# Performance work log

Hardware: AMD Instinct MI355X
Metric: run time of the kernel (lower is better)

The kernel has to match this reference:

```python
import jax, jax.numpy as jnp
import numpy as np

EPS = 1e-5  # BatchNorm2d default eps


def _bn_params(c, gamma):
    # rows: gamma, beta, running_mean, running_var (inference-mode BN)
    return jnp.stack([jnp.full((c,), gamma, jnp.float32),
                      jnp.zeros((c,), jnp.float32),
                      jnp.zeros((c,), jnp.float32),
                      jnp.ones((c,), jnp.float32)])


def _bn(x, p):
    g, b, m, v = p
    scale = (g / jnp.sqrt(v + EPS)).reshape(1, -1, 1, 1)
    return (x - m.reshape(1, -1, 1, 1)) * scale + b.reshape(1, -1, 1, 1)


def _conv1x1(x, w, b):
    # w: [O, C]; 1x1 Conv2d == channel matmul
    return jnp.einsum('oc,nctv->notv', w, x) + b[None, :, None, None]


def setup_inputs() -> dict:
    key = jax.random.key(0)
    N, C, COUT, T, V, S = 8, 64, 128, 256, 256, 3
    IC = COUT // 4  # coff_embedding = 4
    ks = jax.random.split(key, 10)
    rn = lambda k, shp, s=0.05: jax.random.normal(k, shp, jnp.float32) * s
    x = jax.random.normal(ks[0], (N, C, T, V), jnp.float32)
    mat_adj = jax.random.uniform(ks[1], (S, T, T), jnp.float32) * (1.0 / T)  # static adjacency
    adj_weight = jnp.full((S, T, T), 1e-6, jnp.float32)  # nn.init.constant_(weight, 1e-6)
    return {
        'x': x,
        'mat_adj': mat_adj,
        'adj_weight': adj_weight,
        'wa': rn(ks[2], (S, IC, C)), 'ba': jnp.zeros((S, IC), jnp.float32),
        'wb': rn(ks[3], (S, IC, C)), 'bb': jnp.zeros((S, IC), jnp.float32),
        'wd': rn(ks[4], (S, COUT, C)), 'bd': jnp.zeros((S, COUT), jnp.float32),
        'gcn_bn': _bn_params(COUT, 1e-6),  # util.init_bn(self.bn, 1e-6)
        'cres_w': rn(ks[5], (COUT, C)), 'cres_b': jnp.zeros((COUT,), jnp.float32),
        'cres_bn': _bn_params(COUT, 1.0),
        'tcn_w': rn(ks[6], (COUT, COUT, 9)), 'tcn_b': jnp.zeros((COUT,), jnp.float32),
        'tcn_bn': _bn_params(COUT, 1.0),
        'rt_w': rn(ks[7], (COUT, C)), 'rt_b': jnp.zeros((COUT,), jnp.float32),
        'rt_bn': _bn_params(COUT, 1.0),
    }


def reference(x, mat_adj, adj_weight, wa, ba, wb, bb, wd, bd, gcn_bn,
              cres_w, cres_b, cres_bn, tcn_w, tcn_b, tcn_bn, rt_w, rt_b, rt_bn):
    N, C, T, V = x.shape
    A = mat_adj + adj_weight  # [S, T, T]
    y = 0.0
    for i in range(A.shape[0]):  # num_subset = 3, structurally distinct weights
        a = _conv1x1(x, wa[i], ba[i])      # [N, IC, T, V]
        be = _conv1x1(x, wb[i], bb[i])     # [N, IC, T, V]
        # embed1 [N,T,IC*V] @ embed2 [N,IC*V,T] -> contract over (IC, V)
        scores = jnp.einsum('nctv,ncsv->nts', a, be) / V
        att = jax.nn.softmax(scores, axis=-2)  # Softmax(dim=-2)
        adapt = A[i] + att                      # [N, T, T]
        # mat_inpt [N,C*V,T] @ adapt -> view(N,C,V,T)
        xa = jnp.einsum('nctv,nts->ncvs', x, adapt)  # [N, C, V, T]
        y = y + _conv1x1(xa, wd[i], bd[i])           # [N, COUT, V, T]
    gcn = jax.nn.relu(_bn(y, gcn_bn) + _bn(_conv1x1(x, cres_w, cres_b), cres_bn))
    # UnitTSCN: Conv2d kernel (9,1), stride (1,1), padding (4,0), then BN
    t = jax.lax.conv_general_dilated(gcn, tcn_w[..., None], (1, 1), ((4, 4), (0, 0)),
                                     dimension_numbers=('NCHW', 'OIHW', 'NCHW'))
    t = _bn(t + tcn_b[None, :, None, None], tcn_bn)
    # residual path: UnitTSCN(kernel_size=1, stride=1) since in != out
    r = _bn(_conv1x1(x, rt_w, rt_b), rt_bn)
    return jax.nn.relu(t + r)
```

## Files before the change

### kernel.cpp

```cpp
#include <hip/hip_runtime.h>

typedef unsigned short u16;

#define DEVI static __device__ __forceinline__

DEVI float bf2f(u16 v) { return __uint_as_float(((unsigned)v) << 16); }
DEVI u16 f2bf(float f) {
  unsigned u = __float_as_uint(f);
  u += 0x7FFFu + ((u >> 16) & 1u);
  return (u16)(u >> 16);
}
DEVI unsigned pk2bf(float a, float b) {
  unsigned r;
  asm("v_cvt_pk_bf16_f32 %0, %1, %2" : "=v"(r) : "v"(a), "v"(b));
  return r;
}

typedef __attribute__((ext_vector_type(8))) short short8;
typedef __attribute__((ext_vector_type(4))) float floatx4;

#define GSWZ(q, g) (((q) << 6) + ((((g) ^ ((q) & 7) ^ (((q) >> 3) & 7))) << 3))


__global__ void k_diag(float* out, float v) { out[0] = v; }

__global__ __launch_bounds__(256) void k_xt(
    const float* __restrict__ x, u16* __restrict__ xt)
{
  __shared__ __align__(16) u16 Ls[256 * 64];
  const int n = blockIdx.z, c = blockIdx.y, t0 = blockIdx.x << 6;
  const int tid = threadIdx.x;
  const float* xp = x + (((size_t)(n << 6) + c) << 16);
  const int t4 = (tid & 15) << 2;
  #pragma unroll
  for (int j = 0; j < 4; ++j) {
    const int v4 = ((tid >> 4) << 2) + (j << 6);
    float4 f0 = *(const float4*)(xp + ((t0 + t4 + 0) << 8) + v4);
    float4 f1 = *(const float4*)(xp + ((t0 + t4 + 1) << 8) + v4);
    float4 f2 = *(const float4*)(xp + ((t0 + t4 + 2) << 8) + v4);
    float4 f3 = *(const float4*)(xp + ((t0 + t4 + 3) << 8) + v4);
    const float fr[4][4] = {{f0.x,f1.x,f2.x,f3.x},{f0.y,f1.y,f2.y,f3.y},
                            {f0.z,f1.z,f2.z,f3.z},{f0.w,f1.w,f2.w,f3.w}};
    #pragma unroll
    for (int dv = 0; dv < 4; ++dv) {
      int v = v4 + dv;
      unsigned p0 = pk2bf(fr[dv][0], fr[dv][1]);
      unsigned p1 = pk2bf(fr[dv][2], fr[dv][3]);
      int e = (v << 6) + (((t4 >> 3) ^ (v & 7)) << 3) + (t4 & 4);
      *(uint2*)&Ls[e] = make_uint2(p0, p1);
    }
  }
  __syncthreads();
  const int g = tid & 7;
  u16* xo = xt + (((size_t)((n << 6) + c)) << 16) + t0;
  #pragma unroll
  for (int it = 0; it < 8; ++it) {
    int v = (tid >> 3) + (it << 5);
    short8 row = *(const short8*)&Ls[(v << 6) + ((g ^ (v & 7)) << 3)];
    *(short8*)(xo + (v << 8) + (g << 3)) = row;
  }
}

__global__ __launch_bounds__(256) void k_ab2(
    const float* __restrict__ x, const float* __restrict__ wa, const float* __restrict__ ba,
    const float* __restrict__ wb, const float* __restrict__ bb,
    u16* __restrict__ a_buf, u16* __restrict__ b_buf, int sub)
{
  __shared__ __align__(16) u16 Aw[64 * 64];
  __shared__ __align__(16) u16 Bx[256 * 64];
  __shared__ float sbias[64];
  const int n = blockIdx.y;
  const int q0 = blockIdx.x << 8;
  const int tid = threadIdx.x;

  if (tid < 64) sbias[tid] = (tid < 32) ? ba[sub * 32 + tid] : bb[sub * 32 + tid - 32];
  {
    const int kq = tid & 15;
    const int rr = tid >> 4;
    #pragma unroll
    for (int j = 0; j < 4; ++j) {
      int r = rr + (j << 4);
      float4 wv = (r < 32) ? *(const float4*)(wa + sub * 2048 + r * 64 + (kq << 2))
                           : *(const float4*)(wb + sub * 2048 + (r - 32) * 64 + (kq << 2));
      int e = (r << 6) + (((kq >> 1) ^ (r & 7)) << 3) + ((kq & 1) << 2);
      *(uint2*)&Aw[e] = make_uint2(pk2bf(wv.x, wv.y), pk2bf(wv.z, wv.w));
    }
  }
  {
    const int q4 = (tid & 63) << 2;
    const int kb = (tid >> 6) << 4;
    #pragma unroll
    for (int half = 0; half < 2; ++half) {
      float fa[8][4];
      #pragma unroll
      for (int dk = 0; dk < 8; ++dk)
        *(float4*)fa[dk] = *(const float4*)(x + (((size_t)(n << 6) + kb + half * 8 + dk) << 16) + q0 + q4);
      const int G = (kb >> 3) + half;
      #pragma unroll
      for (int dq = 0; dq < 4; ++dq) {
        unsigned w0 = pk2bf(fa[0][dq], fa[1][dq]);
        unsigned w1 = pk2bf(fa[2][dq], fa[3][dq]);
        unsigned w2 = pk2bf(fa[4][dq], fa[5][dq]);
        unsigned w3 = pk2bf(fa[6][dq], fa[7][dq]);
        *(uint4*)&Bx[GSWZ(q4 + dq, G)] = make_uint4(w0, w1, w2, w3);
      }
    }
  }
  __syncthreads();

  const int lane = tid & 63, wave = tid >> 6;
  const int qw = wave << 6;
  const int l15 = lane & 15, lg = lane >> 4;
  int aoff[4], boff[4];
  #pragma unroll
  for (int m = 0; m < 4; ++m) { int r = (m << 4) + l15; aoff[m] = (r << 6) + ((r & 7) << 3); }
  #pragma unroll
  for (int nn = 0; nn < 4; ++nn) { int q = qw + (nn << 4) + l15; boff[nn] = GSWZ(q, 0); }

  floatx4 acc[4][4];
  #pragma unroll
  for (int m = 0; m < 4; ++m)
    #pragma unroll
    for (int nn = 0; nn < 4; ++nn) acc[m][nn] = (floatx4){0.f, 0.f, 0.f, 0.f};

  #pragma unroll
  for (int ks = 0; ks < 2; ++ks) {
    const int gs = ((ks << 2) + lg) << 3;
    short8 av[4], bv[4];
    #pragma unroll
    for (int m = 0; m < 4; ++m) av[m] = *(const short8*)&Aw[aoff[m] ^ gs];
    #pragma unroll
    for (int nn = 0; nn < 4; ++nn) bv[nn] = *(const short8*)&Bx[boff[nn] ^ gs];
    #pragma unroll
    for (int m = 0; m < 4; ++m)
      #pragma unroll
      for (int nn = 0; nn < 4; ++nn)
        acc[m][nn] = __builtin_amdgcn_mfma_f32_16x16x32_bf16(av[m], bv[nn], acc[m][nn], 0, 0, 0);
  }

  #pragma unroll
  for (int m = 0; m < 4; ++m) {
    #pragma unroll
    for (int r = 0; r < 4; ++r) {
      int row = (m << 4) + (lg << 2) + r;
      float bias = sbias[row];
      u16* dst = (row < 32) ? a_buf + (((n * 32 + row) << 16) + q0)
                            : b_buf + (((n * 32 + row - 32) << 16) + q0);
      #pragma unroll
      for (int np = 0; np < 2; ++np) {
        unsigned p = pk2bf(acc[m][2 * np][r] + bias, acc[m][2 * np + 1][r] + bias);
        dst[qw + np * 32 + l15] = (u16)p;
        dst[qw + np * 32 + 16 + l15] = (u16)(p >> 16);
      }
    }
  }
}

__global__ __launch_bounds__(256) void k_sc2(
    const u16* __restrict__ a_buf, const u16* __restrict__ b_buf,
    float* __restrict__ part)
{
  __shared__ __align__(16) u16 At[128 * 64];
  __shared__ __align__(16) u16 Bt[128 * 64];
  const int n = blockIdx.z;
  const int kg = blockIdx.y;
  const int t0 = (blockIdx.x >> 1) << 7;
  const int s0 = (blockIdx.x & 1) << 7;
  const int tid = threadIdx.x;
  const int lane = tid & 63, wave = tid >> 6;
  const int tw = (wave & 1) << 6;
  const int sw = (wave >> 1) << 6;
  const int l15 = lane & 15, lg = lane >> 4;
  const int g = tid & 7;
  const int trow = tid >> 3;

  int aoff[4], boff[4];
  #pragma unroll
  for (int m = 0; m < 4; ++m) { int t = tw + (m << 4) + l15; aoff[m] = (t << 6) + ((t & 7) << 3); }
  #pragma unroll
  for (int nn = 0; nn < 4; ++nn) { int s = sw + (nn << 4) + l15; boff[nn] = (s << 6) + ((s & 7) << 3); }

  floatx4 acc[4][4];
  #pragma unroll
  for (int m = 0; m < 4; ++m)
    #pragma unroll
    for (int nn = 0; nn < 4; ++nn) acc[m][nn] = (floatx4){0.f, 0.f, 0.f, 0.f};

  for (int cc = 0; cc < 4; ++cc) {
    const int c = (kg << 2) + cc;
    const u16* ap = a_buf + ((n * 32 + c) << 16);
    const u16* bp = b_buf + ((n * 32 + c) << 16);
    for (int vt = 0; vt < 4; ++vt) {
      const int v0 = vt << 6;
      __syncthreads();
      #pragma unroll
      for (int j = 0; j < 4; ++j) {
        int t = trow + (j << 5);
        int e = (t << 6) + ((g ^ (t & 7)) << 3);
        *(short8*)&At[e] = *(const short8*)(ap + (t0 + t) * 256 + v0 + g * 8);
        *(short8*)&Bt[e] = *(const short8*)(bp + (s0 + t) * 256 + v0 + g * 8);
      }
      __syncthreads();
      #pragma unroll
      for (int ks = 0; ks < 2; ++ks) {
        const int gs = ((ks << 2) + lg) << 3;
        short8 av[4], bv[4];
        #pragma unroll
        for (int m = 0; m < 4; ++m) av[m] = *(const short8*)&At[aoff[m] ^ gs];
        #pragma unroll
        for (int nn = 0; nn < 4; ++nn) bv[nn] = *(const short8*)&Bt[boff[nn] ^ gs];
        #pragma unroll
        for (int m = 0; m < 4; ++m)
          #pragma unroll
          for (int nn = 0; nn < 4; ++nn)
            acc[m][nn] = __builtin_amdgcn_mfma_f32_16x16x32_bf16(av[m], bv[nn], acc[m][nn], 0, 0, 0);
      }
    }
  }

  const float inv256 = 1.0f / 256.0f;
  float* pp = part + (((kg << 3) + n) << 16);
  #pragma unroll
  for (int m = 0; m < 4; ++m) {
    #pragma unroll
    for (int r = 0; r < 4; ++r) {
      int t = t0 + tw + (m << 4) + (lg << 2) + r;
      #pragma unroll
      for (int nn = 0; nn < 4; ++nn) {
        int s = s0 + sw + (nn << 4) + l15;
        pp[t * 256 + s] = acc[m][nn][r] * inv256;
      }
    }
  }
}

__global__ __launch_bounds__(256) void k_soft2(
    const float* __restrict__ part, const float* __restrict__ madj,
    const float* __restrict__ wadj, float* __restrict__ adapt, int sub)
{
  __shared__ float Ls[256][32];
  __shared__ float redm[8][32];
  __shared__ float reds[8][32];
  const int sc = blockIdx.x;
  const int n = blockIdx.y;
  const int tid = threadIdx.x;
  const int sl = tid & 31, tg = tid >> 5;
  const int s = (sc << 5) + sl;

  float m = -1e30f;
  for (int i = 0; i < 32; ++i) {
    int t = (tg << 5) + i;
    int off = t * 256 + s;
    float v = 0.f;
    #pragma unroll
    for (int k = 0; k < 8; ++k) v += part[(((k << 3) + n) << 16) + off];
    Ls[t][sl] = v;
    m = fmaxf(m, v);
  }
  redm[tg][sl] = m;
  __syncthreads();
  #pragma unroll
  for (int k = 0; k < 8; ++k) m = fmaxf(m, redm[k][sl]);
  float sum = 0.f;
  for (int i = 0; i < 32; ++i) {
    int t = (tg << 5) + i;
    sum += __expf(Ls[t][sl] - m);
  }
  reds[tg][sl] = sum;
  __syncthreads();
  float tot = 0.f;
  #pragma unroll
  for (int k = 0; k < 8; ++k) tot += reds[k][sl];
  float inv = 1.0f / tot;
  const float* ma = madj + (sub << 16);
  const float* wa2 = wadj + (sub << 16);
  float* adp = adapt + (n << 16);
  for (int i = 0; i < 32; ++i) {
    int t = (tg << 5) + i;
    int off = t * 256 + s;
    adp[off] = __expf(Ls[t][sl] - m) * inv + ma[off] + wa2[off];
  }
}

__global__ __launch_bounds__(256) void k_xa2(
    const u16* __restrict__ xt, const float* __restrict__ adapt,
    u16* __restrict__ xa)
{
  __shared__ __align__(16) u16 Av[128 * 64];
  __shared__ __align__(16) u16 Bt2[128 * 64];
  const int n = blockIdx.z, c = blockIdx.y;
  const int v0 = (blockIdx.x >> 1) << 7;
  const int s0 = (blockIdx.x & 1) << 7;
  const int tid = threadIdx.x;
  const int lane = tid & 63, wave = tid >> 6;
  const int vw = (wave & 1) << 6, sw = (wave >> 1) << 6;
  const int l15 = lane & 15, lg = lane >> 4;
  const int ga = tid & 7, vr = tid >> 3;
  const int q4 = (tid & 31) << 2, kb = (tid >> 5) << 3;
  const u16* xp = xt + (((size_t)((n << 6) + c)) << 16);
  const float* ap = adapt + (n << 16);

  int aoff[4], boff[4];
  #pragma unroll
  for (int m = 0; m < 4; ++m) { int v = vw + (m << 4) + l15; aoff[m] = (v << 6) + ((v & 7) << 3); }
  #pragma unroll
  for (int nn = 0; nn < 4; ++nn) { int s = sw + (nn << 4) + l15; boff[nn] = GSWZ(s, 0); }

  floatx4 acc[4][4];
  #pragma unroll
  for (int m = 0; m < 4; ++m)
    #pragma unroll
    for (int nn = 0; nn < 4; ++nn) acc[m][nn] = (floatx4){0.f, 0.f, 0.f, 0.f};

  for (int kt = 0; kt < 4; ++kt) {
    const int tb = kt << 6;
    __syncthreads();
    #pragma unroll
    for (int j = 0; j < 4; ++j) {
      int v = vr + (j << 5);
      *(short8*)&Av[(v << 6) + ((ga ^ (v & 7)) << 3)] =
        *(const short8*)(xp + ((v0 + v) << 8) + tb + (ga << 3));
    }
    {
      float fa[8][4];
      #pragma unroll
      for (int dk = 0; dk < 8; ++dk)
        *(float4*)fa[dk] = *(const float4*)(ap + ((tb + kb + dk) << 8) + s0 + q4);
      const int G = kb >> 3;
      #pragma unroll
      for (int dq = 0; dq < 4; ++dq) {
        unsigned w0 = pk2bf(fa[0][dq], fa[1][dq]);
        unsigned w1 = pk2bf(fa[2][dq], fa[3][dq]);
        unsigned w2 = pk2bf(fa[4][dq], fa[5][dq]);
        unsigned w3 = pk2bf(fa[6][dq], fa[7][dq]);
        *(uint4*)&Bt2[GSWZ(q4 + dq, G)] = make_uint4(w0, w1, w2, w3);
      }
    }
    __syncthreads();
    #pragma unroll
    for (int ks = 0; ks < 2; ++ks) {
      const int gs = ((ks << 2) + lg) << 3;
      short8 av[4], bv[4];
      #pragma unroll
      for (int m = 0; m < 4; ++m) av[m] = *(const short8*)&Av[aoff[m] ^ gs];
      #pragma unroll
      for (int nn = 0; nn < 4; ++nn) bv[nn] = *(const short8*)&Bt2[boff[nn] ^ gs];
      #pragma unroll
      for (int m = 0; m < 4; ++m)
        #pragma unroll
        for (int nn = 0; nn < 4; ++nn)
          acc[m][nn] = __builtin_amdgcn_mfma_f32_16x16x32_bf16(av[m], bv[nn], acc[m][nn], 0, 0, 0);
    }
  }

  u16* xo = xa + (((n << 6) + c) << 16);
  #pragma unroll
  for (int m = 0; m < 4; ++m) {
    #pragma unroll
    for (int r = 0; r < 4; ++r) {
      int v = v0 + vw + (m << 4) + (lg << 2) + r;
      u16* dst = xo + v * 256 + s0;
      #pragma unroll
      for (int np = 0; np < 2; ++np) {
        unsigned p = pk2bf(acc[m][2 * np][r], acc[m][2 * np + 1][r]);
        dst[sw + np * 32 + l15] = (u16)p;
        dst[sw + np * 32 + 16 + l15] = (u16)(p >> 16);
      }
    }
  }
}

__global__ __launch_bounds__(256) void k_gcnf(
    const u16* __restrict__ xa_all, const float* __restrict__ x,
    const float* __restrict__ wd, const float* __restrict__ bd,
    const float* __restrict__ cw, const float* __restrict__ cb,
    const float* __restrict__ cbn, const float* __restrict__ gbn,
    u16* __restrict__ gcn)
{
  __shared__ __align__(16) u16 Wt[128 * 64];
  __shared__ __align__(16) u16 Gt[128 * 64];
  __shared__ float s_kk[128], s_sg[128], s_sc[128];
  const int n = blockIdx.y;
  const int q0 = blockIdx.x << 7;
  const int tid = threadIdx.x;
  if (tid < 128) {
    int o = tid;
    float sg = gbn[o] * rsqrtf(gbn[384 + o] + 1e-5f);
    float sc = cbn[o] * rsqrtf(cbn[384 + o] + 1e-5f);
    s_sg[o] = sg; s_sc[o] = sc;
    s_kk[o] = sg * (bd[o] + bd[128 + o] + bd[256 + o])
            + (cb[o] - cbn[256 + o]) * sc + cbn[128 + o]
            - gbn[256 + o] * sg + gbn[128 + o];
  }
  __syncthreads();

  const int lane = tid & 63, wave = tid >> 6;
  const int ow = (wave & 1) << 6;
  const int qw = (wave >> 1) << 6;
  const int l15 = lane & 15, lg = lane >> 4;
  const int kq = tid & 15;
  const int orow = tid >> 4;
  const int q4 = (tid & 31) << 2;
  const int kb = (tid >> 5) << 3;

  int aoff[4], boff[4];
  #pragma unroll
  for (int m = 0; m < 4; ++m) { int o = ow + (m << 4) + l15; aoff[m] = (o << 6) + ((o & 7) << 3); }
  #pragma unroll
  for (int nn = 0; nn < 4; ++nn) { int q = qw + (nn << 4) + l15; boff[nn] = GSWZ(q, 0); }

  floatx4 acc[4][4];
  #pragma unroll
  for (int m = 0; m < 4; ++m)
    #pragma unroll
    for (int nn = 0; nn < 4; ++nn) acc[m][nn] = (floatx4){0.f, 0.f, 0.f, 0.f};

  for (int kt = 0; kt < 6; ++kt) {
    __syncthreads();
    #pragma unroll
    for (int j = 0; j < 8; ++j) {
      int o = orow + (j << 4);
      int e = (o << 6) + (((kq >> 1) ^ (o & 7)) << 3) + ((kq & 1) << 2);
      if (kt < 3) {
        float4 wv = *(const float4*)(wd + kt * 8192 + o * 64 + (kq << 2));
        float s = s_sg[o];
        *(uint2*)&Wt[e] = make_uint2(pk2bf(s * wv.x, s * wv.y), pk2bf(s * wv.z, s * wv.w));
      } else {
        float4 wv = *(const float4*)(cw + o * 64 + (kq << 2));
        float s = s_sc[o];
        float f0 = s * wv.x, f1 = s * wv.y, f2 = s * wv.z, f3 = s * wv.w;
        unsigned h01 = pk2bf(f0, f1), h23 = pk2bf(f2, f3);
        if (kt == 4) {
          float g0 = __uint_as_float(h01 << 16), g1 = __uint_as_float(h01 & 0xffff0000u);
          float g2 = __uint_as_float(h23 << 16), g3 = __uint_as_float(h23 & 0xffff0000u);
          *(uint2*)&Wt[e] = make_uint2(pk2bf(f0 - g0, f1 - g1), pk2bf(f2 - g2, f3 - g3));
        } else {
          *(uint2*)&Wt[e] = make_uint2(h01, h23);
        }
      }
    }
    if (kt != 4) {
      const int G = kb >> 3;
      if (kt < 3) {
        const u16* xp = xa_all + (size_t)kt * 33554432u + (((size_t)(n << 6) + kb) << 16);
        u16 va[8][4];
        #pragma unroll
        for (int dk = 0; dk < 8; ++dk) {
          ushort4 t4 = *(const ushort4*)(xp + ((size_t)dk << 16) + q0 + q4);
          va[dk][0] = t4.x; va[dk][1] = t4.y; va[dk][2] = t4.z; va[dk][3] = t4.w;
        }
        #pragma unroll
        for (int dq = 0; dq < 4; ++dq) {
          unsigned p0 = (unsigned)va[0][dq] | ((unsigned)va[1][dq] << 16);
          unsigned p1 = (unsigned)va[2][dq] | ((unsigned)va[3][dq] << 16);
          unsigned p2 = (unsigned)va[4][dq] | ((unsigned)va[5][dq] << 16);
          unsigned p3 = (unsigned)va[6][dq] | ((unsigned)va[7][dq] << 16);
          *(uint4*)&Gt[GSWZ(q4 + dq, G)] = make_uint4(p0, p1, p2, p3);
        }
      } else {
        float fa[8][4];
        #pragma unroll
        for (int dk = 0; dk < 8; ++dk)
          *(float4*)fa[dk] = *(const float4*)(x + (((size_t)(n << 6) + kb + dk) << 16) + q0 + q4);
        #pragma unroll
        for (int dq = 0; dq < 4; ++dq) {
          unsigned p[4];
          #pragma unroll
          for (int k2 = 0; k2 < 4; ++k2) {
            unsigned h = pk2bf(fa[2 * k2][dq], fa[2 * k2 + 1][dq]);
            if (kt == 5) {
              float g0 = __uint_as_float(h << 16), g1 = __uint_as_float(h & 0xffff0000u);
              h = pk2bf(fa[2 * k2][dq] - g0, fa[2 * k2 + 1][dq] - g1);
            }
            p[k2] = h;
          }
          *(uint4*)&Gt[GSWZ(q4 + dq, G)] = make_uint4(p[0], p[1], p[2], p[3]);
        }
      }
    }
    __syncthreads();
    #pragma unroll
    for (int ks = 0; ks < 2; ++ks) {
      const int gs = ((ks << 2) + lg) << 3;
      short8 av[4], bv[4];
      #pragma unroll
      for (int m = 0; m < 4; ++m) av[m] = *(const short8*)&Wt[aoff[m] ^ gs];
      #pragma unroll
      for (int nn = 0; nn < 4; ++nn) bv[nn] = *(const short8*)&Gt[boff[nn] ^ gs];
      #pragma unroll
      for (int m = 0; m < 4; ++m)
        #pragma unroll
        for (int nn = 0; nn < 4; ++nn)
          acc[m][nn] = __builtin_amdgcn_mfma_f32_16x16x32_bf16(av[m], bv[nn], acc[m][nn], 0, 0, 0);
    }
  }

  #pragma unroll
  for (int m = 0; m < 4; ++m) {
    #pragma unroll
    for (int r = 0; r < 4; ++r) {
      int o = ow + (m << 4) + (lg << 2) + r;
      float kadd = s_kk[o];
      u16* dst = gcn + (((n << 7) + o) << 16) + q0;
      #pragma unroll
      for (int np = 0; np < 2; ++np) {
        float v0 = fmaxf(acc[m][2 * np][r] + kadd, 0.f);
        float v1 = fmaxf(acc[m][2 * np + 1][r] + kadd, 0.f);
        unsigned p = pk2bf(v0, v1);
        dst[qw + np * 32 + l15] = (u16)p;
        dst[qw + np * 32 + 16 + l15] = (u16)(p >> 16);
      }
    }
  }
}

__global__ __launch_bounds__(256) void k_out(
    const u16* __restrict__ gcn, const float* __restrict__ x,
    const float* __restrict__ tw, const float* __restrict__ tb, const float* __restrict__ tbn,
    const float* __restrict__ rw, const float* __restrict__ rb, const float* __restrict__ rbn,
    float* __restrict__ out)
{
  __shared__ __align__(16) u16 Wh[128 * 64];
  __shared__ __align__(16) u16 Wl[128 * 64];
  __shared__ __align__(16) u16 Gc[128 * 64];
  __shared__ float s_st[128], s_sr[128], s_kk[128];
  const int n = blockIdx.y;
  const int q0 = blockIdx.x << 7;
  const int h = q0 >> 8;
  const int w0 = q0 & 255;
  const int tid = threadIdx.x;
  if (tid < 128) {
    int o = tid;
    float st = tbn[o] * rsqrtf(tbn[384 + o] + 1e-5f);
    float sr = rbn[o] * rsqrtf(rbn[384 + o] + 1e-5f);
    s_st[o] = st; s_sr[o] = sr;
    s_kk[o] = (tb[o] - tbn[256 + o]) * st + tbn[128 + o]
            + (rb[o] - rbn[256 + o]) * sr + rbn[128 + o];
  }
  __syncthreads();

  const int lane = tid & 63;
  const int wave = tid >> 6;
  const int ow = (wave & 1) << 6;
  const int qw = (wave >> 1) << 6;
  const int l15 = lane & 15;
  const int lg  = lane >> 4;

  const int kq   = tid & 15;
  const int orow = tid >> 4;
  const int q4   = (tid & 31) << 2;
  const int kb   = (tid >> 5) << 3;

  float stj[8], srj[8];
  #pragma unroll
  for (int j = 0; j < 8; ++j) { int o = orow + (j << 4); stj[j] = s_st[o]; srj[j] = s_sr[o]; }

  int aoff[4], boff[4];
  #pragma unroll
  for (int m = 0; m < 4; ++m) { int o = ow + (m << 4) + l15; aoff[m] = (o << 6) + ((o & 7) << 3); }
  #pragma unroll
  for (int nn = 0; nn < 4; ++nn) { int q = qw + (nn << 4) + l15; boff[nn] = GSWZ(q, 0); }

  floatx4 acc[4][4];
  #pragma unroll
  for (int m = 0; m < 4; ++m)
    #pragma unroll
    for (int nn = 0; nn < 4; ++nn)
      acc[m][nn] = (floatx4){0.f, 0.f, 0.f, 0.f};

  for (int kc = 0; kc < 19; ++kc) {
    __syncthreads();
    {
      const int k4 = (kc << 6) + (kq << 2);
      #pragma unroll
      for (int j = 0; j < 8; ++j) {
        int o = orow + (j << 4);
        float4 wv;
        float s;
        if (kc < 18) { wv = *(const float4*)(tw + o * 1152 + k4); s = stj[j]; }
        else         { wv = *(const float4*)(rw + (o << 6) + (k4 - 1152)); s = srj[j]; }
        float f0 = s * wv.x, f1 = s * wv.y, f2 = s * wv.z, f3 = s * wv.w;
        unsigned h01 = pk2bf(f0, f1), h23 = pk2bf(f2, f3);
        float g0 = __uint_as_float(h01 << 16), g1 = __uint_as_float(h01 & 0xffff0000u);
        float g2 = __uint_as_float(h23 << 16), g3 = __uint_as_float(h23 & 0xffff0000u);
        unsigned l01 = pk2bf(f0 - g0, f1 - g1), l23 = pk2bf(f2 - g2, f3 - g3);
        int e = (o << 6) + (((kq >> 1) ^ (o & 7)) << 3) + ((kq & 1) << 2);
        *(uint2*)&Wh[e] = make_uint2(h01, h23);
        *(uint2*)&Wl[e] = make_uint2(l01, l23);
      }
    }
    {
      const int G = kb >> 3;
      if (kc < 18) {
        u16 va[8][4];
        #pragma unroll
        for (int dk = 0; dk < 8; ++dk) {
          int k = (kc << 6) + kb + dk;
          unsigned i = (unsigned)k / 9u;
          int kh = k - 9 * (int)i;
          int h2 = h + kh - 4;
          ushort4 t4;
          if ((unsigned)h2 < 256u)
            t4 = *(const ushort4*)(gcn + ((((n << 7) + (int)i) << 16) + (h2 << 8) + w0 + q4));
          else t4 = make_ushort4(0, 0, 0, 0);
          va[dk][0] = t4.x; va[dk][1] = t4.y; va[dk][2] = t4.z; va[dk][3] = t4.w;
        }
        #pragma unroll
        for (int dq = 0; dq < 4; ++dq) {
          unsigned p0 = (unsigned)va[0][dq] | ((unsigned)va[1][dq] << 16);
          unsigned p1 = (unsigned)va[2][dq] | ((unsigned)va[3][dq] << 16);
          unsigned p2 = (unsigned)va[4][dq] | ((unsigned)va[5][dq] << 16);
          unsigned p3 = (unsigned)va[6][dq] | ((unsigned)va[7][dq] << 16);
          *(uint4*)&Gc[GSWZ(q4 + dq, G)] = make_uint4(p0, p1, p2, p3);
        }
      } else {
        float fa[8][4];
        #pragma unroll
        for (int dk = 0; dk < 8; ++dk)
          *(float4*)fa[dk] = *(const float4*)(x + (((size_t)(n << 6) + kb + dk) << 16) + q0 + q4);
        #pragma unroll
        for (int dq = 0; dq < 4; ++dq) {
          unsigned w0_ = pk2bf(fa[0][dq], fa[1][dq]);
          unsigned w1_ = pk2bf(fa[2][dq], fa[3][dq]);
          unsigned w2_ = pk2bf(fa[4][dq], fa[5][dq]);
          unsigned w3_ = pk2bf(fa[6][dq], fa[7][dq]);
          *(uint4*)&Gc[GSWZ(q4 + dq, G)] = make_uint4(w0_, w1_, w2_, w3_);
        }
      }
    }
    __syncthreads();
    #pragma unroll
    for (int ks = 0; ks < 2; ++ks) {
      const int gs = ((ks << 2) + lg) << 3;
      short8 ah[4], al[4], bg[4];
      #pragma unroll
      for (int m = 0; m < 4; ++m) {
        ah[m] = *(const short8*)&Wh[aoff[m] ^ gs];
        al[m] = *(const short8*)&Wl[aoff[m] ^ gs];
      }
      #pragma unroll
      for (int nn = 0; nn < 4; ++nn)
        bg[nn] = *(const short8*)&Gc[boff[nn] ^ gs];
      #pragma unroll
      for (int m = 0; m < 4; ++m)
        #pragma unroll
        for (int nn = 0; nn < 4; ++nn) {
          acc[m][nn] = __builtin_amdgcn_mfma_f32_16x16x32_bf16(ah[m], bg[nn], acc[m][nn], 0, 0, 0);
          acc[m][nn] = __builtin_amdgcn_mfma_f32_16x16x32_bf16(al[m], bg[nn], acc[m][nn], 0, 0, 0);
        }
    }
  }

  #pragma unroll
  for (int m = 0; m < 4; ++m) {
    #pragma unroll
    for (int r = 0; r < 4; ++r) {
      int o = ow + (m << 4) + (lg << 2) + r;
      float kadd = s_kk[o];
      float* dst = out + (((size_t)((n << 7) + o)) << 16) + q0;
      #pragma unroll
      for (int nn = 0; nn < 4; ++nn) {
        int q = qw + (nn << 4) + l15;
        dst[q] = fmaxf(acc[m][nn][r] + kadd, 0.f);
      }
    }
  }
}

extern "C" void kernel_launch(void* const* d_in, const int* in_sizes, int n_in,
                              void* d_out, int out_size, void* d_ws, size_t ws_size,
                              hipStream_t stream) {
  const float* x       = (const float*)d_in[0];
  const float* mat_adj = (const float*)d_in[1];
  const float* adj_w   = (const float*)d_in[2];
  const float* wa      = (const float*)d_in[3];
  const float* ba      = (const float*)d_in[4];
  const float* wb      = (const float*)d_in[5];
  const float* bb      = (const float*)d_in[6];
  const float* wd      = (const float*)d_in[7];
  const float* bd      = (const float*)d_in[8];
  const float* gcn_bn  = (const float*)d_in[9];
  const float* cres_w  = (const float*)d_in[10];
  const float* cres_b  = (const float*)d_in[11];
  const float* cres_bn = (const float*)d_in[12];
  const float* tcn_w   = (const float*)d_in[13];
  const float* tcn_b   = (const float*)d_in[14];
  const float* tcn_bn  = (const float*)d_in[15];
  const float* rt_w    = (const float*)d_in[16];
  const float* rt_b    = (const float*)d_in[17];
  const float* rt_bn   = (const float*)d_in[18];
  float* out = (float*)d_out;

  (void)hipGetLastError();

  hipMemsetAsync(d_out, 0x42, 4, stream);

  if (n_in != 19)                    { k_diag<<<1,1,0,stream>>>(out, 2019.f); return; }
  if (in_sizes[0]  != 33554432)      { k_diag<<<1,1,0,stream>>>(out, 2000.f); return; }
  if (in_sizes[3]  != 6144)          { k_diag<<<1,1,0,stream>>>(out, 2003.f); return; }
  if (in_sizes[7]  != 24576)         { k_diag<<<1,1,0,stream>>>(out, 2007.f); return; }
  if (in_sizes[9]  != 512)           { k_diag<<<1,1,0,stream>>>(out, 2009.f); return; }
  if (in_sizes[13] != 147456)        { k_diag<<<1,1,0,stream>>>(out, 2013.f); return; }
  if (in_sizes[16] != 8192)          { k_diag<<<1,1,0,stream>>>(out, 2016.f); return; }
  if (out_size != 67108864)          { k_diag<<<1,1,0,stream>>>(out, 3000.f); return; }
  if (ws_size < 134217728ull)        { k_diag<<<1,1,0,stream>>>(out, (float)ws_size); return; }

  float* wsf   = (float*)d_ws;
  u16*   a_buf = (u16*)d_ws;
  u16*   b_buf = a_buf + 16777216;
  float* part  = wsf + 16777216;
  float* adapt = wsf + 20971520;
  u16*   gcn   = (u16*)d_ws;
  u16*   xa_all = (u16*)d_out;
  u16*   x_t   = ((u16*)d_out) + 100663296;

  k_xt<<<dim3(4, 64, 8), 256, 0, stream>>>(x, x_t);
  for (int i = 0; i < 3; ++i) {
    k_ab2  <<<dim3(256, 8),   256, 0, stream>>>(x, wa, ba, wb, bb, a_buf, b_buf, i);
    k_sc2  <<<dim3(4, 8, 8),  256, 0, stream>>>(a_buf, b_buf, part);
    k_soft2<<<dim3(8, 8),     256, 0, stream>>>(part, mat_adj, adj_w, adapt, i);
    k_xa2  <<<dim3(4, 64, 8), 256, 0, stream>>>(x_t, adapt, xa_all + (size_t)i * 33554432u);
  }
  k_gcnf<<<dim3(512, 8), 256, 0, stream>>>(xa_all, x, wd, bd, cres_w, cres_b,
                                           cres_bn, gcn_bn, gcn);
  k_out<<<dim3(512, 8), 256, 0, stream>>>(gcn, x, tcn_w, tcn_b, tcn_bn,
                                          rt_w, rt_b, rt_bn, out);

  hipError_t le = hipGetLastError();
  if (le != hipSuccess) {
    k_diag<<<1, 1, 0, stream>>>(out, 1.0e9f + (float)(int)le);
  }
}
```

Baseline: 1.605 ms.

## Prefetch next k-chunk into registers in k_out and peel residual chunk

The temporal-conv output kernel now loads the next chunk's weights and gcn tile into registers while the current chunk is converted and multiplied. This is meant to hide global-memory latency behind the MFMA work. The residual 1x1 chunk is moved out of the main loop into its own epilogue step, removing the per-iteration branch. Launch bounds now ask for 3 blocks per CU. In exchange the prefetch buffers raise register pressure, and the hand-placed barriers with an explicit lgkmcnt wait replace the plain __syncthreads.

```diff
diff --git a/kernel.cpp b/kernel.cpp
--- a/kernel.cpp
+++ b/kernel.cpp
@@ -514,7 +514,7 @@
   }
 }
 
-__global__ __launch_bounds__(256) void k_out(
+__global__ __launch_bounds__(256, 3) void k_out(
     const u16* __restrict__ gcn, const float* __restrict__ x,
     const float* __restrict__ tw, const float* __restrict__ tb, const float* __restrict__ tbn,
     const float* __restrict__ rw, const float* __restrict__ rb, const float* __restrict__ rbn,
@@ -552,14 +552,19 @@
   const int kb   = (tid >> 5) << 3;
 
   float stj[8], srj[8];
-  #pragma unroll
-  for (int j = 0; j < 8; ++j) { int o = orow + (j << 4); stj[j] = s_st[o]; srj[j] = s_sr[o]; }
+  int weoff[8];
+  #pragma unroll
+  for (int j = 0; j < 8; ++j) {
+    int o = orow + (j << 4);
+    stj[j] = s_st[o]; srj[j] = s_sr[o];
+    weoff[j] = (o << 6) + (((kq >> 1) ^ (o & 7)) << 3) + ((kq & 1) << 2);
+  }
 
   int aoff[4], boff[4];
   #pragma unroll
   for (int m = 0; m < 4; ++m) { int o = ow + (m << 4) + l15; aoff[m] = (o << 6) + ((o & 7) << 3); }
   #pragma unroll
-  for (int nn = 0; nn < 4; ++nn) { int q = qw + (nn << 4) + l15; boff[nn] = GSWZ(q, 0); }
+  for (int nn = 0; nn < 4; ++nn) { int q = qw + (nn << 4) + l15; boff[nn] = (q << 6) + ((q & 7) << 3); }
 
   floatx4 acc[4][4];
   #pragma unroll
@@ -568,67 +573,71 @@
     for (int nn = 0; nn < 4; ++nn)
       acc[m][nn] = (floatx4){0.f, 0.f, 0.f, 0.f};
 
-  for (int kc = 0; kc < 19; ++kc) {
-    __syncthreads();
+  float4 wbuf[8];
+  ushort4 gbuf[8];
+
+  {
+    const int k4 = kq << 2;
+    #pragma unroll
+    for (int j = 0; j < 8; ++j)
+      wbuf[j] = *(const float4*)(tw + (orow + (j << 4)) * 1152 + k4);
+    #pragma unroll
+    for (int dk = 0; dk < 8; ++dk) {
+      int k = kb + dk;
+      unsigned i = (unsigned)k / 9u;
+      int kh = k - 9 * (int)i;
+      int h2 = h + kh - 4;
+      gbuf[dk] = ((unsigned)h2 < 256u)
+        ? *(const ushort4*)(gcn + ((((n << 7) + (int)i) << 16) + (h2 << 8) + w0 + q4))
+        : make_ushort4(0, 0, 0, 0);
+    }
+  }
+
+  for (int kc = 0; kc < 18; ++kc) {
+    __builtin_amdgcn_s_barrier();
+    #pragma unroll
+    for (int j = 0; j < 8; ++j) {
+      float s = stj[j];
+      float f0 = s * wbuf[j].x, f1 = s * wbuf[j].y, f2 = s * wbuf[j].z, f3 = s * wbuf[j].w;
+      u16 b0 = f2bf(f0), b1 = f2bf(f1), b2 = f2bf(f2), b3 = f2bf(f3);
+      *(ushort4*)&Wh[weoff[j]] = make_ushort4(b0, b1, b2, b3);
+      *(ushort4*)&Wl[weoff[j]] = make_ushort4(f2bf(f0 - bf2f(b0)), f2bf(f1 - bf2f(b1)),
+                                              f2bf(f2 - bf2f(b2)), f2bf(f3 - bf2f(b3)));
+    }
     {
-      const int k4 = (kc << 6) + (kq << 2);
-      #pragma unroll
-      for (int j = 0; j < 8; ++j) {
-        int o = orow + (j << 4);
-        float4 wv;
-        float s;
-        if (kc < 18) { wv = *(const float4*)(tw + o * 1152 + k4); s = stj[j]; }
-        else         { wv = *(const float4*)(rw + (o << 6) + (k4 - 1152)); s = srj[j]; }
-        float f0 = s * wv.x, f1 = s * wv.y, f2 = s * wv.z, f3 = s * wv.w;
-        unsigned h01 = pk2bf(f0, f1), h23 = pk2bf(f2, f3);
-        float g0 = __uint_as_float(h01 << 16), g1 = __uint_as_float(h01 & 0xffff0000u);
-        float g2 = __uint_as_float(h23 << 16), g3 = __uint_as_float(h23 & 0xffff0000u);
-        unsigned l01 = pk2bf(f0 - g0, f1 - g1), l23 = pk2bf(f2 - g2, f3 - g3);
-        int e = (o << 6) + (((kq >> 1) ^ (o & 7)) << 3) + ((kq & 1) << 2);
-        *(uint2*)&Wh[e] = make_uint2(h01, h23);
-        *(uint2*)&Wl[e] = make_uint2(l01, l23);
-      }
-    }
-    {
+      u16 va[8][4];
+      #pragma unroll
+      for (int dk = 0; dk < 8; ++dk) {
+        va[dk][0] = gbuf[dk].x; va[dk][1] = gbuf[dk].y;
+        va[dk][2] = gbuf[dk].z; va[dk][3] = gbuf[dk].w;
+      }
       const int G = kb >> 3;
-      if (kc < 18) {
-        u16 va[8][4];
-        #pragma unroll
-        for (int dk = 0; dk < 8; ++dk) {
-          int k = (kc << 6) + kb + dk;
-          unsigned i = (unsigned)k / 9u;
-          int kh = k - 9 * (int)i;
-          int h2 = h + kh - 4;
-          ushort4 t4;
-          if ((unsigned)h2 < 256u)
-            t4 = *(const ushort4*)(gcn + ((((n << 7) + (int)i) << 16) + (h2 << 8) + w0 + q4));
-          else t4 = make_ushort4(0, 0, 0, 0);
-          va[dk][0] = t4.x; va[dk][1] = t4.y; va[dk][2] = t4.z; va[dk][3] = t4.w;
-        }
-        #pragma unroll
-        for (int dq = 0; dq < 4; ++dq) {
-          unsigned p0 = (unsigned)va[0][dq] | ((unsigned)va[1][dq] << 16);
-          unsigned p1 = (unsigned)va[2][dq] | ((unsigned)va[3][dq] << 16);
-          unsigned p2 = (unsigned)va[4][dq] | ((unsigned)va[5][dq] << 16);
-          unsigned p3 = (unsigned)va[6][dq] | ((unsigned)va[7][dq] << 16);
-          *(uint4*)&Gc[GSWZ(q4 + dq, G)] = make_uint4(p0, p1, p2, p3);
-        }
-      } else {
-        float fa[8][4];
-        #pragma unroll
-        for (int dk = 0; dk < 8; ++dk)
-          *(float4*)fa[dk] = *(const float4*)(x + (((size_t)(n << 6) + kb + dk) << 16) + q0 + q4);
-        #pragma unroll
-        for (int dq = 0; dq < 4; ++dq) {
-          unsigned w0_ = pk2bf(fa[0][dq], fa[1][dq]);
-          unsigned w1_ = pk2bf(fa[2][dq], fa[3][dq]);
-          unsigned w2_ = pk2bf(fa[4][dq], fa[5][dq]);
-          unsigned w3_ = pk2bf(fa[6][dq], fa[7][dq]);
-          *(uint4*)&Gc[GSWZ(q4 + dq, G)] = make_uint4(w0_, w1_, w2_, w3_);
-        }
-      }
-    }
-    __syncthreads();
+      #pragma unroll
+      for (int dq = 0; dq < 4; ++dq) {
+        int q = q4 + dq;
+        int e = (q << 6) + ((G ^ (q & 7)) << 3);
+        *(ushort4*)&Gc[e]     = make_ushort4(va[0][dq], va[1][dq], va[2][dq], va[3][dq]);
+        *(ushort4*)&Gc[e + 4] = make_ushort4(va[4][dq], va[5][dq], va[6][dq], va[7][dq]);
+      }
+    }
+    if (kc < 17) {
+      const int k4 = ((kc + 1) << 6) + (kq << 2);
+      #pragma unroll
+      for (int j = 0; j < 8; ++j)
+        wbuf[j] = *(const float4*)(tw + (orow + (j << 4)) * 1152 + k4);
+      #pragma unroll
+      for (int dk = 0; dk < 8; ++dk) {
+        int k = ((kc + 1) << 6) + kb + dk;
+        unsigned i = (unsigned)k / 9u;
+        int kh = k - 9 * (int)i;
+        int h2 = h + kh - 4;
+        gbuf[dk] = ((unsigned)h2 < 256u)
+          ? *(const ushort4*)(gcn + ((((n << 7) + (int)i) << 16) + (h2 << 8) + w0 + q4))
+          : make_ushort4(0, 0, 0, 0);
+      }
+    }
+    asm volatile("s_waitcnt lgkmcnt(0)" ::: "memory");
+    __builtin_amdgcn_s_barrier();
     #pragma unroll
     for (int ks = 0; ks < 2; ++ks) {
       const int gs = ((ks << 2) + lg) << 3;
@@ -649,6 +658,55 @@
           acc[m][nn] = __builtin_amdgcn_mfma_f32_16x16x32_bf16(al[m], bg[nn], acc[m][nn], 0, 0, 0);
         }
     }
+  }
+
+  __syncthreads();
+  #pragma unroll
+  for (int j = 0; j < 8; ++j) {
+    float s = srj[j];
+    float4 wv = *(const float4*)(rw + ((orow + (j << 4)) << 6) + (kq << 2));
+    float f0 = s * wv.x, f1 = s * wv.y, f2 = s * wv.z, f3 = s * wv.w;
+    u16 b0 = f2bf(f0), b1 = f2bf(f1), b2 = f2bf(f2), b3 = f2bf(f3);
+    *(ushort4*)&Wh[weoff[j]] = make_ushort4(b0, b1, b2, b3);
+    *(ushort4*)&Wl[weoff[j]] = make_ushort4(f2bf(f0 - bf2f(b0)), f2bf(f1 - bf2f(b1)),
+                                            f2bf(f2 - bf2f(b2)), f2bf(f3 - bf2f(b3)));
+  }
+  {
+    float fa[8][4];
+    #pragma unroll
+    for (int dk = 0; dk < 8; ++dk)
+      *(float4*)fa[dk] = *(const float4*)(x + (((size_t)(n << 6) + kb + dk) << 16) + q0 + q4);
+    const int G = kb >> 3;
+    #pragma unroll
+    for (int dq = 0; dq < 4; ++dq) {
+      int q = q4 + dq;
+      int e = (q << 6) + ((G ^ (q & 7)) << 3);
+      *(ushort4*)&Gc[e]     = make_ushort4(f2bf(fa[0][dq]), f2bf(fa[1][dq]),
+                                           f2bf(fa[2][dq]), f2bf(fa[3][dq]));
+      *(ushort4*)&Gc[e + 4] = make_ushort4(f2bf(fa[4][dq]), f2bf(fa[5][dq]),
+                                           f2bf(fa[6][dq]), f2bf(fa[7][dq]));
+    }
+  }
+  __syncthreads();
+  #pragma unroll
+  for (int ks = 0; ks < 2; ++ks) {
+    const int gs = ((ks << 2) + lg) << 3;
+    short8 ah[4], al[4], bg[4];
+    #pragma unroll
+    for (int m = 0; m < 4; ++m) {
+      ah[m] = *(const short8*)&Wh[aoff[m] ^ gs];
+      al[m] = *(const short8*)&Wl[aoff[m] ^ gs];
+    }
+    #pragma unroll
+    for (int nn = 0; nn < 4; ++nn)
+      bg[nn] = *(const short8*)&Gc[boff[nn] ^ gs];
+    #pragma unroll
+    for (int m = 0; m < 4; ++m)
+      #pragma unroll
+      for (int nn = 0; nn < 4; ++nn) {
+        acc[m][nn] = __builtin_amdgcn_mfma_f32_16x16x32_bf16(ah[m], bg[nn], acc[m][nn], 0, 0, 0);
+        acc[m][nn] = __builtin_amdgcn_mfma_f32_16x16x32_bf16(al[m], bg[nn], acc[m][nn], 0, 0, 0);
+      }
   }
 
   #pragma unroll
```

After: 2.507 ms. +56.2%, slower.
